# Optimization experiments

Hardware: AMD Instinct MI355X
Metric: run time of the kernel (lower is better)

Reference implementation:

```python
import jax, jax.numpy as jnp
import numpy as np
import math

D_MODEL = 1024
N_HEADS = 16
D_K = D_MODEL // N_HEADS


def setup_inputs() -> dict:
    key = jax.random.key(0)
    ks = jax.random.split(key, 5)
    std = math.sqrt(2.0 / (D_MODEL + D_MODEL))
    x = jax.random.normal(ks[0], (2, 2048, D_MODEL), dtype=jnp.float32)
    W_q = jax.random.normal(ks[1], (D_MODEL, D_MODEL), dtype=jnp.float32) * std
    W_k = jax.random.normal(ks[2], (D_MODEL, D_MODEL), dtype=jnp.float32) * std
    W_v = jax.random.normal(ks[3], (D_MODEL, D_MODEL), dtype=jnp.float32) * std
    W_o = jax.random.normal(ks[4], (D_MODEL, D_MODEL), dtype=jnp.float32) * std
    return {"x": x, "W_q": W_q, "W_k": W_k, "W_v": W_v, "W_o": W_o}


def reference(x, W_q, W_k, W_v, W_o):
    B, S, D = x.shape
    H, dk = N_HEADS, D_K
    # projections: (B,S,D) @ (D,D)
    def split_heads(t):  # (B,S,D) -> (B,H,S,dk)
        return t.reshape(B, S, H, dk).transpose(0, 2, 1, 3)
    Q = split_heads(x @ W_q)
    K = split_heads(x @ W_k)
    V = split_heads(x @ W_v)
    scale = 1.0 / math.sqrt(dk)
    scores = jnp.einsum("bhqd,bhkd->bhqk", Q, K) * scale  # (B,H,S,S)
    attn = jax.nn.softmax(scores, axis=-1)
    out = jnp.einsum("bhqk,bhkd->bhqd", attn, V)  # (B,H,S,dk)
    concat = out.transpose(0, 2, 1, 3).reshape(B, S, D)
    return concat @ W_o
```

## Files before the change

kernel.cpp:

```cpp
#include <hip/hip_runtime.h>
#include <hip/hip_bf16.h>
#include <math.h>

#define DMODEL 1024
#define NHEADS 16
#define DKH    64
#define BATCH  2
#define SEQ    2048
#define MROWS  (BATCH * SEQ)
#define LOG2E  1.4426950408889634f

typedef __bf16 bf16_t;
typedef bf16_t bf16x8 __attribute__((ext_vector_type(8)));
typedef bf16_t bf16x4 __attribute__((ext_vector_type(4)));
typedef float  floatx4 __attribute__((ext_vector_type(4)));

__device__ __forceinline__ void glds16(const bf16_t* g, bf16_t* l) {
    __builtin_amdgcn_global_load_lds((__attribute__((address_space(1))) unsigned*)(g),
                                     (__attribute__((address_space(3))) unsigned*)(l),
                                     16, 0, 0);
}

__global__ void prep_kernel(const float* __restrict__ x,
                            const float* __restrict__ W0, const float* __restrict__ W1,
                            const float* __restrict__ W2, const float* __restrict__ W3,
                            bf16_t* __restrict__ xb, bf16_t* __restrict__ Wt) {
    __shared__ float t[32][33];
    int bx = blockIdx.x, by = blockIdx.y, z = blockIdx.z;
    int tx = threadIdx.x, ty = threadIdx.y;
    if (z == 0) {
        int tid = ty * 32 + tx;
#pragma unroll
        for (int k = 0; k < 4; ++k) {
            int slot = k * 256 + tid;
            int row = by * 128 + (slot >> 3);
            int col = bx * 32 + (slot & 7) * 4;
            float4 v = *(const float4*)&x[(size_t)row * DMODEL + col];
            bf16x4 o = {(bf16_t)v.x, (bf16_t)v.y, (bf16_t)v.z, (bf16_t)v.w};
            *(bf16x4*)&xb[(size_t)row * DMODEL + col] = o;
        }
        return;
    }
    const float* W = (z == 1) ? W0 : (z == 2) ? W1 : (z == 3) ? W2 : W3;
    bf16_t* dst = Wt + (size_t)(z - 1) * DMODEL * DMODEL;
#pragma unroll
    for (int i = 0; i < 32; i += 8)
        t[ty + i][tx] = W[(size_t)(by * 32 + ty + i) * DMODEL + bx * 32 + tx];
    __syncthreads();
#pragma unroll
    for (int i = 0; i < 32; i += 8)
        dst[(size_t)(bx * 32 + ty + i) * DMODEL + by * 32 + tx] = (bf16_t)t[tx][ty + i];
}

__global__ __launch_bounds__(256) void gemm_qkv_kernel(const bf16_t* __restrict__ A,
                                                       const bf16_t* __restrict__ Bt,
                                                       bf16_t* __restrict__ Qfb,
                                                       bf16_t* __restrict__ Kfb,
                                                       bf16_t* __restrict__ Vfb) {
    __shared__ bf16_t sm[16384];
    bf16_t* As = sm;
    bf16_t* Bs = sm + 8192;
    int tid = threadIdx.x;
    int w = tid >> 6, l = tid & 63, g = l >> 4, lm = l & 15;
    int wr = w >> 1, wc = w & 1;
    int m0 = blockIdx.y * 128, n0 = blockIdx.x * 128;
    int r8 = l >> 3, s8 = l & 7, cw = s8 ^ r8;

    floatx4 acc[4][4];
#pragma unroll
    for (int i = 0; i < 4; ++i)
#pragma unroll
        for (int j = 0; j < 4; ++j) { floatx4 z = {0.f, 0.f, 0.f, 0.f}; acc[i][j] = z; }

    const bf16_t* Ag = A  + (size_t)(m0 + w * 32 + r8) * DMODEL + cw * 8;
    const bf16_t* Bg = Bt + (size_t)(n0 + w * 32 + r8) * DMODEL + cw * 8;

    for (int k0 = 0; k0 < DMODEL; k0 += 64) {
        __syncthreads();
#pragma unroll
        for (int j = 0; j < 4; ++j) {
            glds16(Ag + (size_t)j * 8 * DMODEL + k0, &As[(w * 32 + j * 8) * 64]);
            glds16(Bg + (size_t)j * 8 * DMODEL + k0, &Bs[(w * 32 + j * 8) * 64]);
        }
        __syncthreads();
#pragma unroll
        for (int kk = 0; kk < 2; ++kk) {
            bf16x8 af[4], bfr[4];
            int c = kk * 4 + g;
            int sw = (c ^ (lm & 7)) * 8;
#pragma unroll
            for (int i = 0; i < 4; ++i) {
                af[i]  = *(const bf16x8*)&As[(wr * 64 + i * 16 + lm) * 64 + sw];
                bfr[i] = *(const bf16x8*)&Bs[(wc * 64 + i * 16 + lm) * 64 + sw];
            }
#pragma unroll
            for (int i = 0; i < 4; ++i)
#pragma unroll
                for (int j = 0; j < 4; ++j)
                    acc[i][j] = __builtin_amdgcn_mfma_f32_16x16x32_bf16(af[i], bfr[j], acc[i][j], 0, 0, 0);
        }
    }

    __syncthreads();
    int mat = n0 >> 10;
    int headb = (n0 & 1023) >> 6;
    int b = m0 >> 11;
    int ktb = (m0 & 2047) >> 6;

    if (mat == 0) {
        const float scale = 0.125f * LOG2E;
#pragma unroll
        for (int i = 0; i < 4; ++i)
#pragma unroll
            for (int j = 0; j < 4; ++j) {
                int d = j * 16 + lm;
                int base = (wc * 2 + wr) * 4096 + (i * 2 + (d >> 5)) * 512 + ((d >> 3) & 3) * 128 + (d & 7);
#pragma unroll
                for (int r = 0; r < 4; ++r)
                    sm[base + (g * 4 + r) * 8] = (bf16_t)(acc[i][j][r] * scale);
            }
    } else if (mat == 1) {
#pragma unroll
        for (int i = 0; i < 4; ++i)
#pragma unroll
            for (int j = 0; j < 4; ++j) {
                int d = j * 16 + lm;
                int base = (wc * 2 + wr) * 4096 + ((i >> 1) * 4 + (g & 1) * 2 + (d >> 5)) * 512 +
                           ((d >> 3) & 3) * 128 + ((i & 1) * 8 + (g >> 1) * 4) * 8 + (d & 7);
#pragma unroll
                for (int r = 0; r < 4; ++r)
                    sm[base + r * 8] = (bf16_t)acc[i][j][r];
            }
    } else {
#pragma unroll
        for (int i = 0; i < 4; ++i)
#pragma unroll
            for (int j = 0; j < 4; ++j) {
                int base = (wc * 2 + wr) * 4096 + (j * 2 + (i >> 1)) * 512 +
                           (((i & 1) * 2 + (g >> 1)) * 16 + lm) * 8 + (g & 1) * 4;
                bf16x4 pk = {(bf16_t)acc[i][j][0], (bf16_t)acc[i][j][1],
                             (bf16_t)acc[i][j][2], (bf16_t)acc[i][j][3]};
                *(bf16x4*)&sm[base] = pk;
            }
    }
    __syncthreads();
    bf16_t* outbuf = (mat == 0) ? Qfb : (mat == 1) ? Kfb : Vfb;
#pragma unroll
    for (int rep = 0; rep < 8; ++rep) {
        int idx = rep * 256 + tid;
        int c = idx >> 9;
        int off = (idx & 511) * 8;
        int bh2 = b * NHEADS + headb + (c >> 1);
        int kt = ktb + (c & 1);
        *(bf16x8*)(outbuf + ((size_t)bh2 * 32 + kt) * 4096 + off) = *(const bf16x8*)&sm[c * 4096 + off];
    }
}

__global__ __launch_bounds__(256) void gemmO_kernel(const bf16_t* __restrict__ A,
                                                    const bf16_t* __restrict__ Bt,
                                                    float* __restrict__ outp) {
    __shared__ bf16_t As[64 * 64];
    __shared__ bf16_t Bs[128 * 64];
    int tid = threadIdx.x;
    int w = tid >> 6, l = tid & 63, g = l >> 4, lm = l & 15;
    int wr = w & 1, wc = w >> 1;
    int m0 = blockIdx.y * 64, n0 = blockIdx.x * 128;
    int r8 = l >> 3, s8 = l & 7, cw = s8 ^ r8;

    floatx4 acc[2][4];
#pragma unroll
    for (int i = 0; i < 2; ++i)
#pragma unroll
        for (int j = 0; j < 4; ++j) { floatx4 z = {0.f, 0.f, 0.f, 0.f}; acc[i][j] = z; }

    const bf16_t* Ag = A  + (size_t)(m0 + w * 16 + r8) * DMODEL + cw * 8;
    const bf16_t* Bg = Bt + (size_t)(n0 + w * 32 + r8) * DMODEL + cw * 8;

    for (int k0 = 0; k0 < DMODEL; k0 += 64) {
        __syncthreads();
#pragma unroll
        for (int j = 0; j < 2; ++j)
            glds16(Ag + (size_t)j * 8 * DMODEL + k0, &As[(w * 16 + j * 8) * 64]);
#pragma unroll
        for (int j = 0; j < 4; ++j)
            glds16(Bg + (size_t)j * 8 * DMODEL + k0, &Bs[(w * 32 + j * 8) * 64]);
        __syncthreads();
#pragma unroll
        for (int kk = 0; kk < 2; ++kk) {
            bf16x8 af[2], bfr[4];
            int c = kk * 4 + g;
            int sw = (c ^ (lm & 7)) * 8;
#pragma unroll
            for (int i = 0; i < 2; ++i)
                af[i] = *(const bf16x8*)&As[(wr * 32 + i * 16 + lm) * 64 + sw];
#pragma unroll
            for (int j = 0; j < 4; ++j)
                bfr[j] = *(const bf16x8*)&Bs[(wc * 64 + j * 16 + lm) * 64 + sw];
#pragma unroll
            for (int i = 0; i < 2; ++i)
#pragma unroll
                for (int j = 0; j < 4; ++j)
                    acc[i][j] = __builtin_amdgcn_mfma_f32_16x16x32_bf16(af[i], bfr[j], acc[i][j], 0, 0, 0);
        }
    }

#pragma unroll
    for (int i = 0; i < 2; ++i)
#pragma unroll
        for (int j = 0; j < 4; ++j) {
            int nc = n0 + wc * 64 + j * 16 + lm;
            int mb = m0 + wr * 32 + i * 16 + g * 4;
#pragma unroll
            for (int r = 0; r < 4; ++r)
                outp[(size_t)(mb + r) * DMODEL + nc] = acc[i][j][r];
        }
}

__global__ __launch_bounds__(256, 2) void attn_kernel(const bf16_t* __restrict__ Qf,
                                                      const bf16_t* __restrict__ Kf,
                                                      const bf16_t* __restrict__ Vf,
                                                      bf16_t* __restrict__ Cc) {
    __shared__ __align__(16) char smem[24576];
    float*  Mbuf = (float*)smem;
    float*  Lbuf = (float*)(smem + 20480);
    bf16_t* Ct   = (bf16_t*)(smem + 21504);

    int tid = threadIdx.x;
    int w = tid >> 6, l = tid & 63, g = l >> 4, lm = l & 15;
    int bh = blockIdx.x, b = bh >> 4, h = bh & 15;
    int q0 = blockIdx.y * 64;

    const bf16_t* Qfh = Qf + ((size_t)bh * 32 + (q0 >> 6)) * 4096 + l * 8;
    const bf16_t* Kfh = Kf + (size_t)bh * 32 * 4096 + l * 8;
    const bf16_t* Vfh = Vf + (size_t)bh * 32 * 4096 + l * 8;

    bf16x8 qf[4][2];
#pragma unroll
    for (int nt = 0; nt < 4; ++nt)
#pragma unroll
        for (int kk = 0; kk < 2; ++kk)
            qf[nt][kk] = *(const bf16x8*)(Qfh + (nt * 2 + kk) * 512);

    floatx4 oacc[4][4];
#pragma unroll
    for (int dt = 0; dt < 4; ++dt)
#pragma unroll
        for (int nt = 0; nt < 4; ++nt) { floatx4 z = {0.f, 0.f, 0.f, 0.f}; oacc[dt][nt] = z; }
    float lsum[4] = {0.f, 0.f, 0.f, 0.f};

    int kt0 = w * 8;
    bf16x8 kfa[2][2], kfb[2][2], vfa[4], vfb[4];
    {
        const bf16_t* Kb0 = Kfh + (size_t)kt0 * 4096;
#pragma unroll
        for (int c = 0; c < 2; ++c)
#pragma unroll
            for (int kk = 0; kk < 2; ++kk)
                kfa[c][kk] = *(const bf16x8*)(Kb0 + (c * 2 + kk) * 512);
    }

    for (int it = 0; it < 8; ++it) {
        const bf16_t* Tb = Kfh + (size_t)(kt0 + it) * 4096;
        const bf16_t* Vb = Vfh + (size_t)(kt0 + it) * 4096;
        const bf16_t* Tn = Kfh + (size_t)(kt0 + ((it < 7) ? it + 1 : 0)) * 4096;

#pragma unroll
        for (int dt = 0; dt < 4; ++dt) vfa[dt] = *(const bf16x8*)(Vb + (dt * 2 + 0) * 512);
#pragma unroll
        for (int c = 0; c < 2; ++c)
#pragma unroll
            for (int kk = 0; kk < 2; ++kk)
                kfb[c][kk] = *(const bf16x8*)(Tb + (4 + c * 2 + kk) * 512);

        floatx4 sa[2][4];
#pragma unroll
        for (int c = 0; c < 2; ++c)
#pragma unroll
            for (int nt = 0; nt < 4; ++nt) { floatx4 z = {0.f, 0.f, 0.f, 0.f}; sa[c][nt] = z; }
        __builtin_amdgcn_s_setprio(1);
#pragma unroll
        for (int kk = 0; kk < 2; ++kk)
#pragma unroll
            for (int c = 0; c < 2; ++c)
#pragma unroll
                for (int nt = 0; nt < 4; ++nt)
                    sa[c][nt] = __builtin_amdgcn_mfma_f32_16x16x32_bf16(kfa[c][kk], qf[nt][kk], sa[c][nt], 0, 0, 0);
        __builtin_amdgcn_s_setprio(0);

#pragma unroll
        for (int dt = 0; dt < 4; ++dt) vfb[dt] = *(const bf16x8*)(Vb + (dt * 2 + 1) * 512);
#pragma unroll
        for (int c = 0; c < 2; ++c)
#pragma unroll
            for (int kk = 0; kk < 2; ++kk)
                kfa[c][kk] = *(const bf16x8*)(Tn + (c * 2 + kk) * 512);

        floatx4 sb[2][4];
#pragma unroll
        for (int c = 0; c < 2; ++c)
#pragma unroll
            for (int nt = 0; nt < 4; ++nt) { floatx4 z = {0.f, 0.f, 0.f, 0.f}; sb[c][nt] = z; }
        __builtin_amdgcn_s_setprio(1);
#pragma unroll
        for (int kk = 0; kk < 2; ++kk)
#pragma unroll
            for (int c = 0; c < 2; ++c)
#pragma unroll
                for (int nt = 0; nt < 4; ++nt)
                    sb[c][nt] = __builtin_amdgcn_mfma_f32_16x16x32_bf16(kfb[c][kk], qf[nt][kk], sb[c][nt], 0, 0, 0);
        __builtin_amdgcn_s_setprio(0);

        {
            bf16x8 bp[4];
#pragma unroll
            for (int nt = 0; nt < 4; ++nt) {
                float p0 = __builtin_amdgcn_exp2f(sa[0][nt][0]);
                float p1 = __builtin_amdgcn_exp2f(sa[0][nt][1]);
                float p2 = __builtin_amdgcn_exp2f(sa[0][nt][2]);
                float p3 = __builtin_amdgcn_exp2f(sa[0][nt][3]);
                float p4 = __builtin_amdgcn_exp2f(sa[1][nt][0]);
                float p5 = __builtin_amdgcn_exp2f(sa[1][nt][1]);
                float p6 = __builtin_amdgcn_exp2f(sa[1][nt][2]);
                float p7 = __builtin_amdgcn_exp2f(sa[1][nt][3]);
                lsum[nt] += ((p0 + p1) + (p2 + p3)) + ((p4 + p5) + (p6 + p7));
                bf16x8 pk = {(bf16_t)p0, (bf16_t)p1, (bf16_t)p2, (bf16_t)p3,
                             (bf16_t)p4, (bf16_t)p5, (bf16_t)p6, (bf16_t)p7};
                bp[nt] = pk;
            }
            __builtin_amdgcn_s_setprio(1);
#pragma unroll
            for (int dt = 0; dt < 4; ++dt)
#pragma unroll
                for (int nt = 0; nt < 4; ++nt)
                    oacc[dt][nt] = __builtin_amdgcn_mfma_f32_16x16x32_bf16(vfa[dt], bp[nt], oacc[dt][nt], 0, 0, 0);
            __builtin_amdgcn_s_setprio(0);
        }

        {
            bf16x8 bp[4];
#pragma unroll
            for (int nt = 0; nt < 4; ++nt) {
                float p0 = __builtin_amdgcn_exp2f(sb[0][nt][0]);
                float p1 = __builtin_amdgcn_exp2f(sb[0][nt][1]);
                float p2 = __builtin_amdgcn_exp2f(sb[0][nt][2]);
                float p3 = __builtin_amdgcn_exp2f(sb[0][nt][3]);
                float p4 = __builtin_amdgcn_exp2f(sb[1][nt][0]);
                float p5 = __builtin_amdgcn_exp2f(sb[1][nt][1]);
                float p6 = __builtin_amdgcn_exp2f(sb[1][nt][2]);
                float p7 = __builtin_amdgcn_exp2f(sb[1][nt][3]);
                lsum[nt] += ((p0 + p1) + (p2 + p3)) + ((p4 + p5) + (p6 + p7));
                bf16x8 pk = {(bf16_t)p0, (bf16_t)p1, (bf16_t)p2, (bf16_t)p3,
                             (bf16_t)p4, (bf16_t)p5, (bf16_t)p6, (bf16_t)p7};
                bp[nt] = pk;
            }
            __builtin_amdgcn_s_setprio(1);
#pragma unroll
            for (int dt = 0; dt < 4; ++dt)
#pragma unroll
                for (int nt = 0; nt < 4; ++nt)
                    oacc[dt][nt] = __builtin_amdgcn_mfma_f32_16x16x32_bf16(vfb[dt], bp[nt], oacc[dt][nt], 0, 0, 0);
            __builtin_amdgcn_s_setprio(0);
        }
    }

#pragma unroll
    for (int nt = 0; nt < 4; ++nt) {
        float s = lsum[nt];
        s += __shfl_xor(s, 16, 64);
        s += __shfl_xor(s, 32, 64);
        lsum[nt] = s;
    }

    float linv = 0.f;
#pragma unroll
    for (int p = 0; p < 4; ++p) {
        __syncthreads();
#pragma unroll
        for (int nt = 0; nt < 4; ++nt)
            *(floatx4*)&Mbuf[w * 1280 + (nt * 16 + lm) * 20 + g * 4] = oacc[p][nt];
        if (p == 0 && g == 0)
#pragma unroll
            for (int nt = 0; nt < 4; ++nt)
                Lbuf[w * 64 + nt * 16 + lm] = lsum[nt];
        __syncthreads();
        if (p == 0) {
            float lt = 0.f;
#pragma unroll
            for (int w2 = 0; w2 < 4; ++w2)
                lt += Lbuf[w2 * 64 + w * 16 + lm];
            linv = 1.0f / lt;
        }
        {
            floatx4 s = {0.f, 0.f, 0.f, 0.f};
#pragma unroll
            for (int w2 = 0; w2 < 4; ++w2)
                s += *(const floatx4*)&Mbuf[w2 * 1280 + (w * 16 + lm) * 20 + g * 4];
            bf16x4 pk = {(bf16_t)(s[0] * linv), (bf16_t)(s[1] * linv),
                         (bf16_t)(s[2] * linv), (bf16_t)(s[3] * linv)};
            *(bf16x4*)&Ct[w * 384 + lm * 24 + g * 4] = pk;
        }
        {
            int row = l >> 2, dp = l & 3;
            bf16x4 v = *(const bf16x4*)&Ct[w * 384 + row * 24 + dp * 4];
            *(bf16x4*)&Cc[((size_t)(b * SEQ + q0 + w * 16 + row)) * DMODEL + h * DKH + p * 16 + dp * 4] = v;
        }
    }
}

extern "C" void kernel_launch(void* const* d_in, const int* in_sizes, int n_in,
                              void* d_out, int out_size, void* d_ws, size_t ws_size,
                              hipStream_t stream) {
    const float* x  = (const float*)d_in[0];
    const float* Wq = (const float*)d_in[1];
    const float* Wk = (const float*)d_in[2];
    const float* Wv = (const float*)d_in[3];
    const float* Wo = (const float*)d_in[4];

    const size_t NX = (size_t)MROWS * DMODEL;
    const size_t NW = (size_t)DMODEL * DMODEL;
    bf16_t* ws  = (bf16_t*)d_ws;
    bf16_t* xb  = ws;
    bf16_t* Wt  = xb + NX;
    bf16_t* Wto = Wt + 3 * NW;
    bf16_t* Qfb = Wt + 4 * NW;
    bf16_t* Kfb = Qfb + NX;
    bf16_t* Vfb = Kfb + NX;
    bf16_t* Cc  = Vfb + NX;

    prep_kernel<<<dim3(32, 32, 5), dim3(32, 8), 0, stream>>>(x, Wq, Wk, Wv, Wo, xb, Wt);

    gemm_qkv_kernel<<<dim3(3 * DMODEL / 128, MROWS / 128), 256, 0, stream>>>(xb, Wt, Qfb, Kfb, Vfb);

    attn_kernel<<<dim3(BATCH * NHEADS, SEQ / 64), 256, 0, stream>>>(Qfb, Kfb, Vfb, Cc);

    gemmO_kernel<<<dim3(DMODEL / 128, MROWS / 64), 256, 0, stream>>>(Cc, Wto, (float*)d_out);
}
```

Baseline: 173.3 us.

## Rework QKV GEMM into 256x256 tiles with double-buffered phased async loads

The QKV projection GEMM goes from 128x128 tiles with 4 waves to 256x256 tiles with 8 waves, using 128KB of dynamic LDS split into two buffers. Each k-step is cut into four sub-tile MFMA phases, and the next tile's global-to-LDS loads are issued between them, gated by partial vmcnt waits and raw barriers with setprio around the MFMAs. The aim is to hide load latency behind compute and raise operand reuse per LDS byte. In exchange the grid shrinks to 192 blocks at one block per CU, which may underfill the device, and register pressure rises.

```diff
diff --git a/kernel.cpp b/kernel.cpp
--- a/kernel.cpp
+++ b/kernel.cpp
@@ -52,108 +52,165 @@
         dst[(size_t)(bx * 32 + ty + i) * DMODEL + by * 32 + tx] = (bf16_t)t[tx][ty + i];
 }
 
-__global__ __launch_bounds__(256) void gemm_qkv_kernel(const bf16_t* __restrict__ A,
+__global__ __launch_bounds__(512) void gemm_qkv_kernel(const bf16_t* __restrict__ A,
                                                        const bf16_t* __restrict__ Bt,
                                                        bf16_t* __restrict__ Qfb,
                                                        bf16_t* __restrict__ Kfb,
                                                        bf16_t* __restrict__ Vfb) {
-    __shared__ bf16_t sm[16384];
-    bf16_t* As = sm;
-    bf16_t* Bs = sm + 8192;
+    extern __shared__ __align__(16) bf16_t sm[];
     int tid = threadIdx.x;
     int w = tid >> 6, l = tid & 63, g = l >> 4, lm = l & 15;
-    int wr = w >> 1, wc = w & 1;
-    int m0 = blockIdx.y * 128, n0 = blockIdx.x * 128;
-    int r8 = l >> 3, s8 = l & 7, cw = s8 ^ r8;
-
-    floatx4 acc[4][4];
+    int wr = w >> 2, wc = w & 3;
+    int m0 = blockIdx.y * 256, n0 = blockIdx.x * 256;
+
+    int w8l3 = w * 8 + (l >> 3);
+    int cw8  = ((l & 7) ^ (l >> 3)) * 8;
+    const bf16_t* Ag0 = A  + (size_t)m0 * DMODEL;
+    const bf16_t* Bg0 = Bt + (size_t)n0 * DMODEL;
+
+#define STAGE(MATB, LDSB, hh, tt) do {                                             \
+        const bf16_t* _src = (MATB) + (size_t)((hh) * 128 + w8l3) * DMODEL + (tt) * 64 + cw8; \
+        bf16_t* _dst = (LDSB) + (hh) * 8192 + w * 8 * 64;                          \
+        glds16(_src, _dst);                                                        \
+        glds16(_src + (size_t)64 * DMODEL, _dst + 4096);                           \
+    } while (0)
+
+#define PH_SYNC() do { asm volatile("s_waitcnt vmcnt(4)" ::: "memory");            \
+        __builtin_amdgcn_s_barrier(); __builtin_amdgcn_sched_barrier(0); } while (0)
+#define PH_BAR() do { __builtin_amdgcn_s_barrier();                                \
+        __builtin_amdgcn_sched_barrier(0); } while (0)
+
+    floatx4 a00[4][2], a01[4][2], a10[4][2], a11[4][2];
 #pragma unroll
     for (int i = 0; i < 4; ++i)
 #pragma unroll
-        for (int j = 0; j < 4; ++j) { floatx4 z = {0.f, 0.f, 0.f, 0.f}; acc[i][j] = z; }
-
-    const bf16_t* Ag = A  + (size_t)(m0 + w * 32 + r8) * DMODEL + cw * 8;
-    const bf16_t* Bg = Bt + (size_t)(n0 + w * 32 + r8) * DMODEL + cw * 8;
-
-    for (int k0 = 0; k0 < DMODEL; k0 += 64) {
-        __syncthreads();
-#pragma unroll
-        for (int j = 0; j < 4; ++j) {
-            glds16(Ag + (size_t)j * 8 * DMODEL + k0, &As[(w * 32 + j * 8) * 64]);
-            glds16(Bg + (size_t)j * 8 * DMODEL + k0, &Bs[(w * 32 + j * 8) * 64]);
-        }
-        __syncthreads();
-#pragma unroll
-        for (int kk = 0; kk < 2; ++kk) {
-            bf16x8 af[4], bfr[4];
-            int c = kk * 4 + g;
-            int sw = (c ^ (lm & 7)) * 8;
-#pragma unroll
-            for (int i = 0; i < 4; ++i) {
-                af[i]  = *(const bf16x8*)&As[(wr * 64 + i * 16 + lm) * 64 + sw];
-                bfr[i] = *(const bf16x8*)&Bs[(wc * 64 + i * 16 + lm) * 64 + sw];
-            }
-#pragma unroll
-            for (int i = 0; i < 4; ++i)
-#pragma unroll
-                for (int j = 0; j < 4; ++j)
-                    acc[i][j] = __builtin_amdgcn_mfma_f32_16x16x32_bf16(af[i], bfr[j], acc[i][j], 0, 0, 0);
-        }
+        for (int j = 0; j < 2; ++j) {
+            floatx4 z = {0.f, 0.f, 0.f, 0.f};
+            a00[i][j] = z; a01[i][j] = z; a10[i][j] = z; a11[i][j] = z;
+        }
+    bf16x8 af[4][2], bf0[2][2], bf1[2][2];
+
+#define LOAD_AF(ihh, bb) do {                                                      \
+        const bf16_t* _ab = sm + (bb) * 16384 + (ihh) * 8192;                      \
+        _Pragma("unroll")                                                          \
+        for (int i = 0; i < 4; ++i) {                                              \
+            int _hr = (wr * 64 + i * 16 + lm) * 64;                                \
+            af[i][0] = *(const bf16x8*)&_ab[_hr + ((g) ^ (lm & 7)) * 8];           \
+            af[i][1] = *(const bf16x8*)&_ab[_hr + ((4 + g) ^ (lm & 7)) * 8];       \
+        } } while (0)
+
+#define LOAD_BF(BF, jhh, bb) do {                                                  \
+        const bf16_t* _bb = sm + 32768 + (bb) * 16384 + (jhh) * 8192;              \
+        _Pragma("unroll")                                                          \
+        for (int j = 0; j < 2; ++j) {                                              \
+            int _bc = (wc * 32 + j * 16 + lm) * 64;                                \
+            BF[j][0] = *(const bf16x8*)&_bb[_bc + ((g) ^ (lm & 7)) * 8];           \
+            BF[j][1] = *(const bf16x8*)&_bb[_bc + ((4 + g) ^ (lm & 7)) * 8];       \
+        } } while (0)
+
+#define MM(ACC, BF) do {                                                           \
+        __builtin_amdgcn_s_setprio(1);                                             \
+        _Pragma("unroll")                                                          \
+        for (int kk = 0; kk < 2; ++kk)                                             \
+        _Pragma("unroll")                                                          \
+        for (int i = 0; i < 4; ++i)                                                \
+        _Pragma("unroll")                                                          \
+        for (int j = 0; j < 2; ++j)                                                \
+            ACC[i][j] = __builtin_amdgcn_mfma_f32_16x16x32_bf16(af[i][kk], BF[j][kk], ACC[i][j], 0, 0, 0); \
+        __builtin_amdgcn_s_setprio(0);                                             \
+    } while (0)
+
+    STAGE(Ag0, sm, 0, 0);
+    STAGE(Bg0, sm + 32768, 0, 0);
+    STAGE(Bg0, sm + 32768, 1, 0);
+    STAGE(Ag0, sm, 1, 0);
+
+    for (int t = 0; t < 16; ++t) {
+        int buf = t & 1;
+        bf16_t* An = sm + (buf ^ 1) * 16384;
+        bf16_t* Bn = sm + 32768 + (buf ^ 1) * 16384;
+        int tn = (t + 1) & 15;
+
+        PH_SYNC();
+        STAGE(Ag0, An, 0, tn);
+        LOAD_AF(0, buf);
+        LOAD_BF(bf0, 0, buf);
+        MM(a00, bf0);
+        PH_SYNC();
+        STAGE(Bg0, Bn, 0, tn);
+        LOAD_BF(bf1, 1, buf);
+        MM(a01, bf1);
+        PH_SYNC();
+        STAGE(Bg0, Bn, 1, tn);
+        LOAD_AF(1, buf);
+        MM(a11, bf1);
+        PH_BAR();
+        STAGE(Ag0, An, 1, tn);
+        MM(a10, bf0);
     }
 
     __syncthreads();
-    int mat = n0 >> 10;
-    int headb = (n0 & 1023) >> 6;
+    int mat = blockIdx.x >> 2;
+    int headb = (blockIdx.x & 3) * 4;
     int b = m0 >> 11;
     int ktb = (m0 & 2047) >> 6;
-
-    if (mat == 0) {
-        const float scale = 0.125f * LOG2E;
-#pragma unroll
-        for (int i = 0; i < 4; ++i)
-#pragma unroll
-            for (int j = 0; j < 4; ++j) {
-                int d = j * 16 + lm;
-                int base = (wc * 2 + wr) * 4096 + (i * 2 + (d >> 5)) * 512 + ((d >> 3) & 3) * 128 + (d & 7);
-#pragma unroll
-                for (int r = 0; r < 4; ++r)
-                    sm[base + (g * 4 + r) * 8] = (bf16_t)(acc[i][j][r] * scale);
-            }
-    } else if (mat == 1) {
-#pragma unroll
-        for (int i = 0; i < 4; ++i)
-#pragma unroll
-            for (int j = 0; j < 4; ++j) {
-                int d = j * 16 + lm;
-                int base = (wc * 2 + wr) * 4096 + ((i >> 1) * 4 + (g & 1) * 2 + (d >> 5)) * 512 +
-                           ((d >> 3) & 3) * 128 + ((i & 1) * 8 + (g >> 1) * 4) * 8 + (d & 7);
-#pragma unroll
-                for (int r = 0; r < 4; ++r)
-                    sm[base + r * 8] = (bf16_t)acc[i][j][r];
-            }
-    } else {
-#pragma unroll
-        for (int i = 0; i < 4; ++i)
-#pragma unroll
-            for (int j = 0; j < 4; ++j) {
-                int base = (wc * 2 + wr) * 4096 + (j * 2 + (i >> 1)) * 512 +
-                           (((i & 1) * 2 + (g >> 1)) * 16 + lm) * 8 + (g & 1) * 4;
-                bf16x4 pk = {(bf16_t)acc[i][j][0], (bf16_t)acc[i][j][1],
-                             (bf16_t)acc[i][j][2], (bf16_t)acc[i][j][3]};
-                *(bf16x4*)&sm[base] = pk;
-            }
-    }
+    const float scaleQ = 0.125f * LOG2E;
+
+#define EPI(ACC, ihh, jhh)                                                          \
+    _Pragma("unroll")                                                               \
+    for (int i = 0; i < 4; ++i)                                                     \
+    _Pragma("unroll")                                                               \
+    for (int j = 0; j < 2; ++j) {                                                   \
+        int s0_ = (ihh) * 128 + wr * 64 + i * 16 + g * 4;                           \
+        int d_  = (jhh) * 128 + wc * 32 + j * 16 + lm;                              \
+        int hc_ = d_ >> 6, d6 = d_ & 63, st_ = s0_ >> 6, s6 = s0_ & 63;             \
+        int chunk = hc_ * 4 + st_;                                                  \
+        if (mat == 0) {                                                             \
+            int base = chunk * 4096 + ((s6 >> 4) * 2 + (d6 >> 5)) * 512 +           \
+                       ((d6 >> 3) & 3) * 128 + (s6 & 15) * 8 + (d6 & 7);            \
+            _Pragma("unroll")                                                       \
+            for (int r = 0; r < 4; ++r)                                             \
+                sm[base + r * 8] = (bf16_t)(ACC[i][j][r] * scaleQ);                 \
+        } else if (mat == 1) {                                                      \
+            int base = chunk * 4096 + (((s6 >> 5) & 1) * 4 + ((s6 >> 2) & 1) * 2 + (d6 >> 5)) * 512 + \
+                       ((d6 >> 3) & 3) * 128 +                                      \
+                       (((s6 >> 4) & 1) * 8 + ((s6 >> 3) & 1) * 4) * 8 + (d6 & 7);  \
+            _Pragma("unroll")                                                       \
+            for (int r = 0; r < 4; ++r)                                             \
+                sm[base + r * 8] = (bf16_t)ACC[i][j][r];                            \
+        } else {                                                                    \
+            int base = chunk * 4096 + ((d6 >> 4) * 2 + ((s6 >> 5) & 1)) * 512 +     \
+                       ((((s6 >> 4) & 1) * 2 + ((s6 >> 3) & 1)) * 16 + (d6 & 15)) * 8 + \
+                       ((s6 >> 2) & 1) * 4;                                         \
+            bf16x4 pk = {(bf16_t)ACC[i][j][0], (bf16_t)ACC[i][j][1],                \
+                         (bf16_t)ACC[i][j][2], (bf16_t)ACC[i][j][3]};               \
+            *(bf16x4*)&sm[base] = pk;                                               \
+        }                                                                           \
+    }
+
+    EPI(a00, 0, 0);
+    EPI(a01, 0, 1);
+    EPI(a10, 1, 0);
+    EPI(a11, 1, 1);
+
     __syncthreads();
     bf16_t* outbuf = (mat == 0) ? Qfb : (mat == 1) ? Kfb : Vfb;
 #pragma unroll
-    for (int rep = 0; rep < 8; ++rep) {
-        int idx = rep * 256 + tid;
+    for (int rep = 0; rep < 16; ++rep) {
+        int idx = rep * 512 + tid;
         int c = idx >> 9;
         int off = (idx & 511) * 8;
-        int bh2 = b * NHEADS + headb + (c >> 1);
-        int kt = ktb + (c & 1);
+        int bh2 = b * NHEADS + headb + (c >> 2);
+        int kt = ktb + (c & 3);
         *(bf16x8*)(outbuf + ((size_t)bh2 * 32 + kt) * 4096 + off) = *(const bf16x8*)&sm[c * 4096 + off];
     }
+#undef STAGE
+#undef PH_SYNC
+#undef PH_BAR
+#undef LOAD_AF
+#undef LOAD_BF
+#undef MM
+#undef EPI
 }
 
 __global__ __launch_bounds__(256) void gemmO_kernel(const bf16_t* __restrict__ A,
@@ -429,7 +486,7 @@
 
     prep_kernel<<<dim3(32, 32, 5), dim3(32, 8), 0, stream>>>(x, Wq, Wk, Wv, Wo, xb, Wt);
 
-    gemm_qkv_kernel<<<dim3(3 * DMODEL / 128, MROWS / 128), 256, 0, stream>>>(xb, Wt, Qfb, Kfb, Vfb);
+    gemm_qkv_kernel<<<dim3(12, 16), 512, 131072, stream>>>(xb, Wt, Qfb, Kfb, Vfb);
 
     attn_kernel<<<dim3(BATCH * NHEADS, SEQ / 64), 256, 0, stream>>>(Qfb, Kfb, Vfb, Cc);
 
```

Result: faster. 165.9 us (-4.3%).
